# Kernel optimization log

Measured on AMD Instinct MI355X. Metric: run time of the kernel, lower is better.

The kernel has to match this reference:

```python
import jax, jax.numpy as jnp
import numpy as np

NUM_PATCHES = 4
PATCH_RADIUS = 0.2


def setup_inputs() -> dict:
    key = jax.random.key(0)
    points = jax.random.normal(key, (64, 65536, 6), dtype=jnp.float32)
    return {"points": points}


def _fps(xyz, n_samples):
    """Furthest point sampling (pointnet2 convention: start at index 0).
    xyz: (B, N, 3) -> (B, n_samples) int32 indices."""
    B, N, _ = xyz.shape

    def body(carry, _):
        min_d, last_idx = carry                                   # (B,N), (B,)
        last = jnp.take_along_axis(xyz, last_idx[:, None, None], axis=1)  # (B,1,3)
        d = jnp.sum((xyz - last) ** 2, axis=-1)                   # (B,N)
        min_d = jnp.minimum(min_d, d)
        nxt = jnp.argmax(min_d, axis=1).astype(jnp.int32)
        return (min_d, nxt), last_idx

    init = (jnp.full((B, N), 1e10, dtype=xyz.dtype),
            jnp.zeros((B,), dtype=jnp.int32))
    (_, _), idxs = jax.lax.scan(body, init, None, length=n_samples)
    return idxs.T                                                  # (B, n_samples)


def reference(points):
    B, N, C = points.shape
    xyz = points[..., :3]

    # 1) pick patch centers via FPS
    centers_idx = _fps(xyz, NUM_PATCHES)                           # (B,P)
    centers = jnp.take_along_axis(xyz, centers_idx[..., None], axis=1)  # (B,P,3)

    # 2) distance of every point to nearest center -> drop mask
    dist = jnp.linalg.norm(xyz[:, :, None, :] - centers[:, None, :, :], axis=-1)  # (B,N,P)
    min_dist = jnp.min(dist, axis=2)                               # (B,N)
    keep = min_dist >= PATCH_RADIUS                                # (B,N) bool, True = kept

    # 3) stable compaction: kept points first (original order preserved),
    #    then repeat-fill pattern valid_points[j % num_valid]
    order = jnp.argsort(jnp.logical_not(keep).astype(jnp.int32), axis=1, stable=True)  # (B,N)
    num_valid = jnp.sum(keep, axis=1)                              # (B,)
    j = jnp.arange(N, dtype=jnp.int32)[None, :]                    # (1,N)
    k = j % jnp.maximum(num_valid, 1)[:, None]                     # (B,N)
    src = jnp.take_along_axis(order, k, axis=1)                    # (B,N)
    out = jnp.take_along_axis(points, src[..., None], axis=1)      # (B,N,C)

    # all points dropped -> zeros (matches torch branch)
    return jnp.where((num_valid > 0)[:, None, None], out, jnp.zeros_like(out))
```

## Files before the change

### kernel.cpp

```cpp
#include <hip/hip_runtime.h>
#include <stdint.h>

#define NN 65536
#define BB 64
#define TPB 256

#define FBPB 32
#define FGRID (BB * FBPB)
#define FPPB 2048
#define FLPT 8

#define GBPB 16
#define GGRID (BB * GBPB)
#define GLPT 16

__device__ __forceinline__ float sqdist(float x, float y, float z,
                                        float cx, float cy, float cz) {
    float dx = __fsub_rn(x, cx);
    float dy = __fsub_rn(y, cy);
    float dz = __fsub_rn(z, cz);
    return __fadd_rn(__fadd_rn(__fmul_rn(dx, dx), __fmul_rn(dy, dy)),
                     __fmul_rn(dz, dz));
}

__device__ __forceinline__ unsigned long long pack_key(float v, int i) {
    return ((unsigned long long)__float_as_uint(v) << 32) |
           (unsigned long long)(0xFFFFFFFFu - (unsigned)i);
}

__device__ __forceinline__ int key_idx(unsigned long long key) {
    return (int)(0xFFFFFFFFu - (unsigned)(key & 0xFFFFFFFFu));
}

__device__ __forceinline__ int reduce_part(const unsigned long long* partKey,
                                           int a, int b) {
    const unsigned long long* s = partKey + a * FGRID + b * FBPB;
    unsigned long long bk = s[0];
    #pragma unroll
    for (int w = 1; w < FBPB; ++w) bk = (s[w] > bk) ? s[w] : bk;
    return key_idx(bk);
}

template<int NC>
__global__ __launch_bounds__(TPB) void fps_pass(
        const float* __restrict__ pts, unsigned long long* partKey) {
    const int gb = blockIdx.x;
    const int b = gb >> 5, blk = gb & 31;
    const int tid = threadIdx.x;
    const int lane = tid & 63, wid = tid >> 6;
    const float* base = pts + (size_t)b * NN * 6;

    float cx[NC], cy[NC], cz[NC];
    cx[0] = base[0]; cy[0] = base[1]; cz[0] = base[2];
    #pragma unroll
    for (int k = 1; k < NC; ++k) {
        int idx = reduce_part(partKey, k - 1, b);
        const float* p = base + (size_t)idx * 6;
        cx[k] = p[0]; cy[k] = p[1]; cz[k] = p[2];
    }

    float bestv = -1.0f; int besti = 0x7fffffff;
    #pragma unroll
    for (int l = 0; l < FLPT; ++l) {
        const int p = blk * FPPB + l * TPB + tid;
        const float* q = base + (size_t)p * 6;
        float2 xy = *(const float2*)q;
        float  zz = q[2];
        float d = sqdist(xy.x, xy.y, zz, cx[0], cy[0], cz[0]);
        #pragma unroll
        for (int k = 1; k < NC; ++k)
            d = fminf(d, sqdist(xy.x, xy.y, zz, cx[k], cy[k], cz[k]));
        if (d > bestv) { bestv = d; besti = p; }
    }
    unsigned long long key = pack_key(bestv, besti);
    #pragma unroll
    for (int off = 32; off > 0; off >>= 1) {
        unsigned long long ok = __shfl_down(key, off, 64);
        if (ok > key) key = ok;
    }
    __shared__ unsigned long long s_k[4];
    if (lane == 0) s_k[wid] = key;
    __syncthreads();
    if (tid == 0) {
        unsigned long long bk = s_k[0];
        #pragma unroll
        for (int w = 1; w < 4; ++w) bk = (s_k[w] > bk) ? s_k[w] : bk;
        partKey[(NC - 1) * FGRID + gb] = bk;
    }
}

__global__ __launch_bounds__(TPB) void fps_final(
        const float* __restrict__ pts,
        const unsigned long long* __restrict__ partKey,
        uint64_t* __restrict__ masks) {
    const int gb = blockIdx.x;
    const int b = gb >> 5, blk = gb & 31;
    const int tid = threadIdx.x;
    const int lane = tid & 63, wid = tid >> 6;
    const float* base = pts + (size_t)b * NN * 6;

    float cx[4], cy[4], cz[4];
    cx[0] = base[0]; cy[0] = base[1]; cz[0] = base[2];
    #pragma unroll
    for (int k = 1; k < 4; ++k) {
        int idx = reduce_part(partKey, k - 1, b);
        const float* p = base + (size_t)idx * 6;
        cx[k] = p[0]; cy[k] = p[1]; cz[k] = p[2];
    }
    uint64_t* mb = masks + (size_t)b * 1024;

    #pragma unroll
    for (int l = 0; l < FLPT; ++l) {
        const int p = blk * FPPB + l * TPB + tid;
        const float* q = base + (size_t)p * 6;
        float2 xy = *(const float2*)q;
        float  zz = q[2];
        float d = sqdist(xy.x, xy.y, zz, cx[0], cy[0], cz[0]);
        #pragma unroll
        for (int k = 1; k < 4; ++k)
            d = fminf(d, sqdist(xy.x, xy.y, zz, cx[k], cy[k], cz[k]));
        int keep = (__fsqrt_rn(d) >= 0.2f) ? 1 : 0;
        uint64_t m = __ballot(keep);
        if (lane == 0) mb[blk * 32 + l * 4 + wid] = m;
    }
}

__global__ __launch_bounds__(TPB) void gather_kernel(
        const float* __restrict__ pts, const uint64_t* __restrict__ masks,
        float* __restrict__ out) {
    const int gb = blockIdx.x;
    const int b = gb >> 4, blk = gb & 15;
    const int tid = threadIdx.x;
    const int lane = tid & 63, wid = tid >> 6;
    __shared__ uint64_t s_m[1024];
    __shared__ int s_pre[1024];
    __shared__ int s_ws[4], s_wo[4];
    __shared__ int s_nv;

    const uint64_t* mb = masks + (size_t)b * 1024;
    uint64_t w[4];
    int cnt = 0;
    #pragma unroll
    for (int k = 0; k < 4; ++k) {
        w[k] = mb[tid * 4 + k];
        s_m[tid * 4 + k] = w[k];
        cnt += __popcll(w[k]);
    }
    int incl = cnt;
    #pragma unroll
    for (int off = 1; off < 64; off <<= 1) {
        int v = __shfl_up(incl, off, 64);
        if (lane >= off) incl += v;
    }
    if (lane == 63) s_ws[wid] = incl;
    __syncthreads();
    if (tid == 0) {
        int run = 0;
        #pragma unroll
        for (int q = 0; q < 4; ++q) { s_wo[q] = run; run += s_ws[q]; }
        s_nv = run;
    }
    __syncthreads();
    int run = s_wo[wid] + incl - cnt;
    #pragma unroll
    for (int k = 0; k < 4; ++k) {
        s_pre[tid * 4 + k] = run;
        run += __popcll(w[k]);
    }
    __syncthreads();

    const int nv = s_nv;
    const float* baseP = pts + (size_t)b * NN * 6;
    float* ob = out + (size_t)b * NN * 6;

    if (nv <= 0) {
        float2 zz = make_float2(0.f, 0.f);
        #pragma unroll
        for (int l = 0; l < GLPT; ++l) {
            int j = blk * 4096 + l * TPB + tid;
            float2* o = (float2*)(ob + (size_t)j * 6);
            o[0] = zz; o[1] = zz; o[2] = zz;
        }
        return;
    }

    #pragma unroll
    for (int l = 0; l < GLPT; ++l) {
        int j = blk * 4096 + l * TPB + tid;
        int jj = (int)((unsigned)j % (unsigned)nv);
        int wd = 0;
        #pragma unroll
        for (int s = 512; s > 0; s >>= 1) {
            int cand = wd + s;
            if (cand < 1024 && s_pre[cand] <= jj) wd = cand;
        }
        int r = jj - s_pre[wd];
        uint64_t m = s_m[wd];
        int bit = 0;
        int c = __popcll(m & 0xFFFFFFFFull);
        if (r >= c) { r -= c; m >>= 32; bit += 32; }
        c = __popcll(m & 0xFFFFull);
        if (r >= c) { r -= c; m >>= 16; bit += 16; }
        c = __popcll(m & 0xFFull);
        if (r >= c) { r -= c; m >>= 8; bit += 8; }
        c = __popcll(m & 0xFull);
        if (r >= c) { r -= c; m >>= 4; bit += 4; }
        c = __popcll(m & 0x3ull);
        if (r >= c) { r -= c; m >>= 2; bit += 2; }
        if (r >= (int)(m & 1ull)) { bit += 1; }
        int src = wd * 64 + bit;
        const float2* p = (const float2*)(baseP + (size_t)src * 6);
        float2* o = (float2*)(ob + (size_t)j * 6);
        float2 r0 = p[0], r1 = p[1], r2 = p[2];
        o[0] = r0; o[1] = r1; o[2] = r2;
    }
}

extern "C" void kernel_launch(void* const* d_in, const int* in_sizes, int n_in,
                              void* d_out, int out_size, void* d_ws, size_t ws_size,
                              hipStream_t stream) {
    const float* pts = (const float*)d_in[0];
    float* out = (float*)d_out;

    unsigned long long* partKey = (unsigned long long*)d_ws;
    uint64_t* masks = (uint64_t*)((char*)d_ws + (64 << 10));

    fps_pass<1><<<FGRID, TPB, 0, stream>>>(pts, partKey);
    fps_pass<2><<<FGRID, TPB, 0, stream>>>(pts, partKey);
    fps_pass<3><<<FGRID, TPB, 0, stream>>>(pts, partKey);
    fps_final<<<FGRID, TPB, 0, stream>>>(pts, partKey, masks);
    gather_kernel<<<GGRID, TPB, 0, stream>>>(pts, masks, out);
}
```

Measured before the change: 247.4 us.

## Fuse FPS passes, mask and gather into one persistent kernel with per-batch barriers

Replaces the five launches with one kernel of 1024 blocks, 16 per batch. Each thread loads its 16 points' xyz into registers once and keeps the running min distance there, instead of re-reading points in every FPS pass. Blocks of the same batch synchronise through atomic spin barriers in the workspace. The kernel relies on all blocks being co-resident, checked via an occupancy query, and falls back to the old multi-kernel path otherwise. The cost is the barrier spin latency and higher register pressure.

```diff
diff --git a/kernel.cpp b/kernel.cpp
--- a/kernel.cpp
+++ b/kernel.cpp
@@ -4,12 +4,16 @@
 #define NN 65536
 #define BB 64
 #define TPB 256
+
+#define BPB 16
+#define GRID_BLKS (BB * BPB)
+#define PPB 4096
+#define LPT 16
 
 #define FBPB 32
 #define FGRID (BB * FBPB)
 #define FPPB 2048
 #define FLPT 8
-
 #define GBPB 16
 #define GGRID (BB * GBPB)
 #define GLPT 16
@@ -30,6 +34,199 @@
 
 __device__ __forceinline__ int key_idx(unsigned long long key) {
     return (int)(0xFFFFFFFFu - (unsigned)(key & 0xFFFFFFFFu));
+}
+
+__device__ __forceinline__ void batch_barrier(unsigned* cnt, unsigned* gen) {
+    __threadfence();
+    __syncthreads();
+    if (threadIdx.x == 0) {
+        unsigned g = __hip_atomic_load(gen, __ATOMIC_RELAXED, __HIP_MEMORY_SCOPE_AGENT);
+        unsigned a = __hip_atomic_fetch_add(cnt, 1u, __ATOMIC_ACQ_REL,
+                                            __HIP_MEMORY_SCOPE_AGENT) + 1u;
+        if (a == (unsigned)BPB) {
+            __hip_atomic_store(cnt, 0u, __ATOMIC_RELAXED, __HIP_MEMORY_SCOPE_AGENT);
+            __hip_atomic_store(gen, g + 1u, __ATOMIC_RELEASE, __HIP_MEMORY_SCOPE_AGENT);
+        } else {
+            while (__hip_atomic_load(gen, __ATOMIC_ACQUIRE,
+                                     __HIP_MEMORY_SCOPE_AGENT) == g)
+                __builtin_amdgcn_s_sleep(2);
+        }
+    }
+    __syncthreads();
+    __threadfence();
+}
+
+__global__ void init_barrier(unsigned* bar) {
+    const int t = threadIdx.x;
+    __hip_atomic_store(&bar[t * 32 + 0], 0u, __ATOMIC_RELAXED, __HIP_MEMORY_SCOPE_AGENT);
+    __hip_atomic_store(&bar[t * 32 + 1], 0u, __ATOMIC_RELAXED, __HIP_MEMORY_SCOPE_AGENT);
+}
+
+__global__ __launch_bounds__(TPB, 4) void fused_kernel(
+        const float* __restrict__ pts,
+        unsigned long long* __restrict__ partKey,
+        uint64_t* __restrict__ masks,
+        float* __restrict__ out,
+        unsigned* __restrict__ bar) {
+    const int gb = blockIdx.x;
+    const int b = gb >> 4, blk = gb & 15;
+    const int tid = threadIdx.x;
+    const int lane = tid & 63, wid = tid >> 6;
+    const float* base = pts + (size_t)b * NN * 6;
+    unsigned* bcnt = bar + b * 32;
+    unsigned* bgen = bar + b * 32 + 1;
+
+    __shared__ unsigned long long s_k[4];
+    __shared__ float s_c[3];
+    __shared__ uint64_t s_m[1024];
+    __shared__ int s_pre[1024];
+    __shared__ int s_ws[4], s_wo[4];
+    __shared__ int s_nv;
+
+    float px[LPT], py[LPT], pz[LPT], md[LPT];
+    #pragma unroll
+    for (int l = 0; l < LPT; ++l) {
+        const int p = blk * PPB + l * TPB + tid;
+        const float* q = base + (size_t)p * 6;
+        float2 xy = *(const float2*)q;
+        px[l] = xy.x; py[l] = xy.y; pz[l] = q[2];
+    }
+
+    float cx = base[0], cy = base[1], cz = base[2];
+    #pragma unroll
+    for (int l = 0; l < LPT; ++l)
+        md[l] = sqdist(px[l], py[l], pz[l], cx, cy, cz);
+
+    for (int k = 0; k < 3; ++k) {
+        float bestv = -1.0f; int besti = 0x7fffffff;
+        #pragma unroll
+        for (int l = 0; l < LPT; ++l) {
+            if (md[l] > bestv) { bestv = md[l]; besti = blk * PPB + l * TPB + tid; }
+        }
+        unsigned long long key = pack_key(bestv, besti);
+        #pragma unroll
+        for (int off = 32; off > 0; off >>= 1) {
+            unsigned long long ok = __shfl_down(key, off, 64);
+            if (ok > key) key = ok;
+        }
+        if (lane == 0) s_k[wid] = key;
+        __syncthreads();
+        if (tid == 0) {
+            unsigned long long bk = s_k[0];
+            #pragma unroll
+            for (int w = 1; w < 4; ++w) bk = (s_k[w] > bk) ? s_k[w] : bk;
+            __hip_atomic_store(&partKey[k * GRID_BLKS + gb], bk,
+                               __ATOMIC_RELAXED, __HIP_MEMORY_SCOPE_AGENT);
+        }
+        batch_barrier(bcnt, bgen);
+
+        if (tid == 0) {
+            const unsigned long long* s = partKey + k * GRID_BLKS + b * BPB;
+            unsigned long long bk = __hip_atomic_load(&s[0], __ATOMIC_RELAXED,
+                                                      __HIP_MEMORY_SCOPE_AGENT);
+            #pragma unroll
+            for (int w = 1; w < BPB; ++w) {
+                unsigned long long v = __hip_atomic_load(&s[w], __ATOMIC_RELAXED,
+                                                         __HIP_MEMORY_SCOPE_AGENT);
+                if (v > bk) bk = v;
+            }
+            const float* cp = base + (size_t)key_idx(bk) * 6;
+            s_c[0] = cp[0]; s_c[1] = cp[1]; s_c[2] = cp[2];
+        }
+        __syncthreads();
+        cx = s_c[0]; cy = s_c[1]; cz = s_c[2];
+        #pragma unroll
+        for (int l = 0; l < LPT; ++l)
+            md[l] = fminf(md[l], sqdist(px[l], py[l], pz[l], cx, cy, cz));
+    }
+
+    uint64_t* mb = masks + (size_t)b * 1024;
+    #pragma unroll
+    for (int l = 0; l < LPT; ++l) {
+        int keep = (__fsqrt_rn(md[l]) >= 0.2f) ? 1 : 0;
+        uint64_t m = __ballot(keep);
+        if (lane == 0)
+            __hip_atomic_store(&mb[blk * 64 + l * 4 + wid], m,
+                               __ATOMIC_RELAXED, __HIP_MEMORY_SCOPE_AGENT);
+    }
+    batch_barrier(bcnt, bgen);
+
+    uint64_t w[4];
+    int cnt = 0;
+    #pragma unroll
+    for (int kk = 0; kk < 4; ++kk) {
+        w[kk] = __hip_atomic_load(&mb[tid * 4 + kk], __ATOMIC_RELAXED,
+                                  __HIP_MEMORY_SCOPE_AGENT);
+        s_m[tid * 4 + kk] = w[kk];
+        cnt += __popcll(w[kk]);
+    }
+    int incl = cnt;
+    #pragma unroll
+    for (int off = 1; off < 64; off <<= 1) {
+        int v = __shfl_up(incl, off, 64);
+        if (lane >= off) incl += v;
+    }
+    if (lane == 63) s_ws[wid] = incl;
+    __syncthreads();
+    if (tid == 0) {
+        int run = 0;
+        #pragma unroll
+        for (int q = 0; q < 4; ++q) { s_wo[q] = run; run += s_ws[q]; }
+        s_nv = run;
+    }
+    __syncthreads();
+    int run = s_wo[wid] + incl - cnt;
+    #pragma unroll
+    for (int kk = 0; kk < 4; ++kk) {
+        s_pre[tid * 4 + kk] = run;
+        run += __popcll(w[kk]);
+    }
+    __syncthreads();
+
+    const int nv = s_nv;
+    float* ob = out + (size_t)b * NN * 6;
+
+    if (nv <= 0) {
+        float2 zz = make_float2(0.f, 0.f);
+        #pragma unroll
+        for (int l = 0; l < LPT; ++l) {
+            int j = blk * PPB + l * TPB + tid;
+            float2* o = (float2*)(ob + (size_t)j * 6);
+            o[0] = zz; o[1] = zz; o[2] = zz;
+        }
+        return;
+    }
+
+    #pragma unroll
+    for (int l = 0; l < LPT; ++l) {
+        int j = blk * PPB + l * TPB + tid;
+        int jj = (int)((unsigned)j % (unsigned)nv);
+        int wd = 0;
+        #pragma unroll
+        for (int s = 512; s > 0; s >>= 1) {
+            int cand = wd + s;
+            if (cand < 1024 && s_pre[cand] <= jj) wd = cand;
+        }
+        int r = jj - s_pre[wd];
+        uint64_t m = s_m[wd];
+        int bit = 0;
+        int c = __popcll(m & 0xFFFFFFFFull);
+        if (r >= c) { r -= c; m >>= 32; bit += 32; }
+        c = __popcll(m & 0xFFFFull);
+        if (r >= c) { r -= c; m >>= 16; bit += 16; }
+        c = __popcll(m & 0xFFull);
+        if (r >= c) { r -= c; m >>= 8; bit += 8; }
+        c = __popcll(m & 0xFull);
+        if (r >= c) { r -= c; m >>= 4; bit += 4; }
+        c = __popcll(m & 0x3ull);
+        if (r >= c) { r -= c; m >>= 2; bit += 2; }
+        if (r >= (int)(m & 1ull)) { bit += 1; }
+        int src = wd * 64 + bit;
+        const float2* p = (const float2*)(base + (size_t)src * 6);
+        float2* o = (float2*)(ob + (size_t)j * 6);
+        float2 r0 = p[0], r1 = p[1], r2 = p[2];
+        o[0] = r0; o[1] = r1; o[2] = r2;
+    }
 }
 
 __device__ __forceinline__ int reduce_part(const unsigned long long* partKey,
@@ -223,11 +420,29 @@
     float* out = (float*)d_out;
 
     unsigned long long* partKey = (unsigned long long*)d_ws;
+    unsigned* bar = (unsigned*)((char*)d_ws + (48 << 10));
     uint64_t* masks = (uint64_t*)((char*)d_ws + (64 << 10));
 
-    fps_pass<1><<<FGRID, TPB, 0, stream>>>(pts, partKey);
-    fps_pass<2><<<FGRID, TPB, 0, stream>>>(pts, partKey);
-    fps_pass<3><<<FGRID, TPB, 0, stream>>>(pts, partKey);
-    fps_final<<<FGRID, TPB, 0, stream>>>(pts, partKey, masks);
-    gather_kernel<<<GGRID, TPB, 0, stream>>>(pts, masks, out);
-}
+    static int fused_ok = -1;
+    if (fused_ok < 0) {
+        int dev = 0;
+        (void)hipGetDevice(&dev);
+        int ncu = 0, nb = 0;
+        hipError_t e1 = hipDeviceGetAttribute(&ncu, hipDeviceAttributeMultiprocessorCount, dev);
+        hipError_t e2 = hipOccupancyMaxActiveBlocksPerMultiprocessor(
+            &nb, (const void*)fused_kernel, TPB, 0);
+        fused_ok = (e1 == hipSuccess && e2 == hipSuccess &&
+                    (long)nb * (long)ncu >= (long)GRID_BLKS) ? 1 : 0;
+    }
+
+    if (fused_ok) {
+        init_barrier<<<1, 64, 0, stream>>>(bar);
+        fused_kernel<<<GRID_BLKS, TPB, 0, stream>>>(pts, partKey, masks, out, bar);
+    } else {
+        fps_pass<1><<<FGRID, TPB, 0, stream>>>(pts, partKey);
+        fps_pass<2><<<FGRID, TPB, 0, stream>>>(pts, partKey);
+        fps_pass<3><<<FGRID, TPB, 0, stream>>>(pts, partKey);
+        fps_final<<<FGRID, TPB, 0, stream>>>(pts, partKey, masks);
+        gather_kernel<<<GGRID, TPB, 0, stream>>>(pts, masks, out);
+    }
+}
```

New measurement: 244.9 us. About the same (-1.0%).

## Convert xyz to SoA and carry running min-distance across FPS passes

Applied to the files above, without the earlier changes.

The first FPS pass now writes x, y, z and the running min-distance into separate planar workspace arrays. Later passes read those arrays with float4 loads and update the stored min-distance against the single new center, instead of rereading the strided 6-float points and recomputing distances to every earlier center. This trades strided 24-byte-stride reads for contiguous reads, but adds a 64 MB write in the init pass and a read-modify-write of the min-distance plane in every middle pass.

```diff
diff --git a/kernel.cpp b/kernel.cpp
--- a/kernel.cpp
+++ b/kernel.cpp
@@ -5,10 +5,10 @@
 #define BB 64
 #define TPB 256
 
-#define FBPB 32
-#define FGRID (BB * FBPB)
-#define FPPB 2048
-#define FLPT 8
+#define BPB 32
+#define FGRID (BB * BPB)
+#define PPB 2048
+#define LPT 8
 
 #define GBPB 16
 #define GGRID (BB * GBPB)
@@ -27,98 +27,149 @@
     return ((unsigned long long)__float_as_uint(v) << 32) |
            (unsigned long long)(0xFFFFFFFFu - (unsigned)i);
 }
-
 __device__ __forceinline__ int key_idx(unsigned long long key) {
     return (int)(0xFFFFFFFFu - (unsigned)(key & 0xFFFFFFFFu));
 }
 
+__device__ __forceinline__ int sel_bit(uint64_t m, int r) {
+    int bit = 0;
+    int c = __popcll(m & 0xFFFFFFFFull);
+    if (r >= c) { r -= c; m >>= 32; bit += 32; }
+    c = __popcll(m & 0xFFFFull);
+    if (r >= c) { r -= c; m >>= 16; bit += 16; }
+    c = __popcll(m & 0xFFull);
+    if (r >= c) { r -= c; m >>= 8; bit += 8; }
+    c = __popcll(m & 0xFull);
+    if (r >= c) { r -= c; m >>= 4; bit += 4; }
+    c = __popcll(m & 0x3ull);
+    if (r >= c) { r -= c; m >>= 2; bit += 2; }
+    if (r >= (int)(m & 1ull)) { bit += 1; }
+    return bit;
+}
+
 __device__ __forceinline__ int reduce_part(const unsigned long long* partKey,
                                            int a, int b) {
-    const unsigned long long* s = partKey + a * FGRID + b * FBPB;
+    const unsigned long long* s = partKey + a * FGRID + b * BPB;
     unsigned long long bk = s[0];
     #pragma unroll
-    for (int w = 1; w < FBPB; ++w) bk = (s[w] > bk) ? s[w] : bk;
+    for (int w = 1; w < BPB; ++w) bk = (s[w] > bk) ? s[w] : bk;
     return key_idx(bk);
 }
 
-template<int NC>
-__global__ __launch_bounds__(TPB) void fps_pass(
-        const float* __restrict__ pts, unsigned long long* partKey) {
+__device__ __forceinline__ void store_partial(float bestv, int besti,
+                                              unsigned long long* slot,
+                                              int tid, int lane, int wid) {
+    unsigned long long key = pack_key(bestv, besti);
+    #pragma unroll
+    for (int off = 32; off > 0; off >>= 1) {
+        unsigned long long ok = __shfl_down(key, off, 64);
+        if (ok > key) key = ok;
+    }
+    __shared__ unsigned long long s_k[4];
+    if (lane == 0) s_k[wid] = key;
+    __syncthreads();
+    if (tid == 0) {
+        unsigned long long bk = s_k[0];
+        #pragma unroll
+        for (int w = 1; w < 4; ++w) bk = (s_k[w] > bk) ? s_k[w] : bk;
+        *slot = bk;
+    }
+}
+
+__global__ __launch_bounds__(TPB) void convert_init(
+        const float* __restrict__ pts,
+        float* __restrict__ X, float* __restrict__ Y,
+        float* __restrict__ Z, float* __restrict__ MD,
+        unsigned long long* __restrict__ partKey) {
     const int gb = blockIdx.x;
     const int b = gb >> 5, blk = gb & 31;
     const int tid = threadIdx.x;
     const int lane = tid & 63, wid = tid >> 6;
     const float* base = pts + (size_t)b * NN * 6;
-
-    float cx[NC], cy[NC], cz[NC];
-    cx[0] = base[0]; cy[0] = base[1]; cz[0] = base[2];
-    #pragma unroll
-    for (int k = 1; k < NC; ++k) {
-        int idx = reduce_part(partKey, k - 1, b);
-        const float* p = base + (size_t)idx * 6;
-        cx[k] = p[0]; cy[k] = p[1]; cz[k] = p[2];
-    }
+    float* Xb = X + (size_t)b * NN;
+    float* Yb = Y + (size_t)b * NN;
+    float* Zb = Z + (size_t)b * NN;
+    float* Mb = MD + (size_t)b * NN;
+
+    const float cx = base[0], cy = base[1], cz = base[2];
 
     float bestv = -1.0f; int besti = 0x7fffffff;
     #pragma unroll
-    for (int l = 0; l < FLPT; ++l) {
-        const int p = blk * FPPB + l * TPB + tid;
+    for (int l = 0; l < LPT; ++l) {
+        const int p = blk * PPB + l * TPB + tid;
         const float* q = base + (size_t)p * 6;
         float2 xy = *(const float2*)q;
         float  zz = q[2];
-        float d = sqdist(xy.x, xy.y, zz, cx[0], cy[0], cz[0]);
-        #pragma unroll
-        for (int k = 1; k < NC; ++k)
-            d = fminf(d, sqdist(xy.x, xy.y, zz, cx[k], cy[k], cz[k]));
+        float d = sqdist(xy.x, xy.y, zz, cx, cy, cz);
+        Xb[p] = xy.x; Yb[p] = xy.y; Zb[p] = zz; Mb[p] = d;
         if (d > bestv) { bestv = d; besti = p; }
     }
-    unsigned long long key = pack_key(bestv, besti);
-    #pragma unroll
-    for (int off = 32; off > 0; off >>= 1) {
-        unsigned long long ok = __shfl_down(key, off, 64);
-        if (ok > key) key = ok;
-    }
-    __shared__ unsigned long long s_k[4];
-    if (lane == 0) s_k[wid] = key;
-    __syncthreads();
-    if (tid == 0) {
-        unsigned long long bk = s_k[0];
-        #pragma unroll
-        for (int w = 1; w < 4; ++w) bk = (s_k[w] > bk) ? s_k[w] : bk;
-        partKey[(NC - 1) * FGRID + gb] = bk;
-    }
-}
-
-__global__ __launch_bounds__(TPB) void fps_final(
-        const float* __restrict__ pts,
+    store_partial(bestv, besti, &partKey[0 * FGRID + gb], tid, lane, wid);
+}
+
+template<int K>
+__global__ __launch_bounds__(TPB) void fps_mid(
+        const float* __restrict__ X, const float* __restrict__ Y,
+        const float* __restrict__ Z, float* __restrict__ MD,
+        unsigned long long* __restrict__ partKey) {
+    const int gb = blockIdx.x;
+    const int b = gb >> 5, blk = gb & 31;
+    const int tid = threadIdx.x;
+    const int lane = tid & 63, wid = tid >> 6;
+    const float* Xb = X + (size_t)b * NN;
+    const float* Yb = Y + (size_t)b * NN;
+    const float* Zb = Z + (size_t)b * NN;
+    float* Mb = MD + (size_t)b * NN;
+
+    const int idx = reduce_part(partKey, K - 1, b);
+    const float cx = Xb[idx], cy = Yb[idx], cz = Zb[idx];
+
+    const int p0 = blk * PPB + tid * 8;
+    float4 x0 = *(const float4*)(Xb + p0), x1 = *(const float4*)(Xb + p0 + 4);
+    float4 y0 = *(const float4*)(Yb + p0), y1 = *(const float4*)(Yb + p0 + 4);
+    float4 z0 = *(const float4*)(Zb + p0), z1 = *(const float4*)(Zb + p0 + 4);
+    float4 m0 = *(const float4*)(Mb + p0), m1 = *(const float4*)(Mb + p0 + 4);
+
+    float xs[8] = {x0.x,x0.y,x0.z,x0.w,x1.x,x1.y,x1.z,x1.w};
+    float ys[8] = {y0.x,y0.y,y0.z,y0.w,y1.x,y1.y,y1.z,y1.w};
+    float zs[8] = {z0.x,z0.y,z0.z,z0.w,z1.x,z1.y,z1.z,z1.w};
+    float ms[8] = {m0.x,m0.y,m0.z,m0.w,m1.x,m1.y,m1.z,m1.w};
+
+    float bestv = -1.0f; int besti = 0x7fffffff;
+    #pragma unroll
+    for (int i = 0; i < 8; ++i) {
+        float d = fminf(ms[i], sqdist(xs[i], ys[i], zs[i], cx, cy, cz));
+        ms[i] = d;
+        if (d > bestv) { bestv = d; besti = p0 + i; }
+    }
+    *(float4*)(Mb + p0)     = make_float4(ms[0], ms[1], ms[2], ms[3]);
+    *(float4*)(Mb + p0 + 4) = make_float4(ms[4], ms[5], ms[6], ms[7]);
+
+    store_partial(bestv, besti, &partKey[K * FGRID + gb], tid, lane, wid);
+}
+
+__global__ __launch_bounds__(TPB) void fps_mask(
+        const float* __restrict__ X, const float* __restrict__ Y,
+        const float* __restrict__ Z, const float* __restrict__ MD,
         const unsigned long long* __restrict__ partKey,
         uint64_t* __restrict__ masks) {
     const int gb = blockIdx.x;
     const int b = gb >> 5, blk = gb & 31;
     const int tid = threadIdx.x;
     const int lane = tid & 63, wid = tid >> 6;
-    const float* base = pts + (size_t)b * NN * 6;
-
-    float cx[4], cy[4], cz[4];
-    cx[0] = base[0]; cy[0] = base[1]; cz[0] = base[2];
-    #pragma unroll
-    for (int k = 1; k < 4; ++k) {
-        int idx = reduce_part(partKey, k - 1, b);
-        const float* p = base + (size_t)idx * 6;
-        cx[k] = p[0]; cy[k] = p[1]; cz[k] = p[2];
-    }
+    const float* Xb = X + (size_t)b * NN;
+    const float* Yb = Y + (size_t)b * NN;
+    const float* Zb = Z + (size_t)b * NN;
+    const float* Mb = MD + (size_t)b * NN;
+
+    const int idx = reduce_part(partKey, 2, b);
+    const float cx = Xb[idx], cy = Yb[idx], cz = Zb[idx];
     uint64_t* mb = masks + (size_t)b * 1024;
 
     #pragma unroll
-    for (int l = 0; l < FLPT; ++l) {
-        const int p = blk * FPPB + l * TPB + tid;
-        const float* q = base + (size_t)p * 6;
-        float2 xy = *(const float2*)q;
-        float  zz = q[2];
-        float d = sqdist(xy.x, xy.y, zz, cx[0], cy[0], cz[0]);
-        #pragma unroll
-        for (int k = 1; k < 4; ++k)
-            d = fminf(d, sqdist(xy.x, xy.y, zz, cx[k], cy[k], cz[k]));
+    for (int l = 0; l < LPT; ++l) {
+        const int p = blk * PPB + l * TPB + tid;
+        float d = fminf(Mb[p], sqdist(Xb[p], Yb[p], Zb[p], cx, cy, cz));
         int keep = (__fsqrt_rn(d) >= 0.2f) ? 1 : 0;
         uint64_t m = __ballot(keep);
         if (lane == 0) mb[blk * 32 + l * 4 + wid] = m;
@@ -194,21 +245,7 @@
             int cand = wd + s;
             if (cand < 1024 && s_pre[cand] <= jj) wd = cand;
         }
-        int r = jj - s_pre[wd];
-        uint64_t m = s_m[wd];
-        int bit = 0;
-        int c = __popcll(m & 0xFFFFFFFFull);
-        if (r >= c) { r -= c; m >>= 32; bit += 32; }
-        c = __popcll(m & 0xFFFFull);
-        if (r >= c) { r -= c; m >>= 16; bit += 16; }
-        c = __popcll(m & 0xFFull);
-        if (r >= c) { r -= c; m >>= 8; bit += 8; }
-        c = __popcll(m & 0xFull);
-        if (r >= c) { r -= c; m >>= 4; bit += 4; }
-        c = __popcll(m & 0x3ull);
-        if (r >= c) { r -= c; m >>= 2; bit += 2; }
-        if (r >= (int)(m & 1ull)) { bit += 1; }
-        int src = wd * 64 + bit;
+        int src = wd * 64 + sel_bit(s_m[wd], jj - s_pre[wd]);
         const float2* p = (const float2*)(baseP + (size_t)src * 6);
         float2* o = (float2*)(ob + (size_t)j * 6);
         float2 r0 = p[0], r1 = p[1], r2 = p[2];
@@ -222,12 +259,18 @@
     const float* pts = (const float*)d_in[0];
     float* out = (float*)d_out;
 
+    const size_t S = (size_t)BB * NN * sizeof(float);
     unsigned long long* partKey = (unsigned long long*)d_ws;
     uint64_t* masks = (uint64_t*)((char*)d_ws + (64 << 10));
-
-    fps_pass<1><<<FGRID, TPB, 0, stream>>>(pts, partKey);
-    fps_pass<2><<<FGRID, TPB, 0, stream>>>(pts, partKey);
-    fps_pass<3><<<FGRID, TPB, 0, stream>>>(pts, partKey);
-    fps_final<<<FGRID, TPB, 0, stream>>>(pts, partKey, masks);
+    char* pb = (char*)d_ws + (1 << 20);
+    float* X  = (float*)(pb);
+    float* Y  = (float*)(pb + S);
+    float* Z  = (float*)(pb + 2 * S);
+    float* MD = (float*)(pb + 3 * S);
+
+    convert_init<<<FGRID, TPB, 0, stream>>>(pts, X, Y, Z, MD, partKey);
+    fps_mid<1><<<FGRID, TPB, 0, stream>>>(X, Y, Z, MD, partKey);
+    fps_mid<2><<<FGRID, TPB, 0, stream>>>(X, Y, Z, MD, partKey);
+    fps_mask<<<FGRID, TPB, 0, stream>>>(X, Y, Z, MD, partKey, masks);
     gather_kernel<<<GGRID, TPB, 0, stream>>>(pts, masks, out);
 }
```

After: 251.4 us. Within noise of the previous version (+1.6%).
